# Performance work log

Hardware: AMD Instinct MI355X
Metric: run time of the kernel (lower is better)

## Reference

```python
import jax, jax.numpy as jnp
import numpy as np

B, T, C, H = 4, 2048, 768, 768  # batch, seq, embed_size, embed_size_h


def setup_inputs() -> dict:
    key = jax.random.key(0)
    ks = jax.random.split(key, 7)
    s = 1.0 / np.sqrt(C)  # torch Linear default-ish init scale
    return {
        "x": jax.random.normal(ks[0], (B, T, C), jnp.float32),
        "Wq": jax.random.normal(ks[1], (C, H), jnp.float32) * s,
        "bq": jnp.zeros((H,), jnp.float32),
        "Wk": jax.random.normal(ks[2], (C, H), jnp.float32) * s,
        "bk": jnp.zeros((H,), jnp.float32),
        "Wv": jax.random.normal(ks[3], (C, H), jnp.float32) * s,
        "bv": jnp.zeros((H,), jnp.float32),
    }


def reference(x, Wq, bq, Wk, bk, Wv, bv):
    # q,k,v: [B,T,H]
    q = x @ Wq + bq
    k = x @ Wk + bk
    v = x @ Wv + bv
    scale = jnp.asarray(H, x.dtype) ** -0.5
    # full [B,T,T] score matrix, as the original module does
    qk = jnp.einsum("btd,bsd->bts", q, k) * scale
    tril = jnp.tril(jnp.ones((T, T), x.dtype))
    qk = qk * tril
    # original quirk: masked_fill on exact zeros (covers upper triangle)
    qk = jnp.where(qk == 0, -jnp.inf, qk)
    attn = jax.nn.softmax(qk, axis=-1)  # [B,T,T]
    # note: in the source, dropout is applied to a dead value; output uses softmax directly
    return attn @ v  # [B,T,H]
```

## Files before the change

### kernel.cpp

```cpp
#include <hip/hip_runtime.h>
#include <math.h>


#define BB 4
#define TT 2048
#define CC 768

typedef __bf16 bf16_t;
typedef __bf16 bf16x8 __attribute__((ext_vector_type(8)));
typedef _Float16 half8 __attribute__((ext_vector_type(8)));
typedef float f32x4 __attribute__((ext_vector_type(4)));

__device__ __forceinline__ void async_load16(void* lds, const void* g) {
  __builtin_amdgcn_global_load_lds(
      (const __attribute__((address_space(1))) void*)g,
      (__attribute__((address_space(3))) void*)lds, 16, 0, 0);
}

__device__ __forceinline__ int swz4(int r) {
  return (r & 3) ^ ((r >> 2) & 3);
}

__device__ __forceinline__ void stage_tile(const bf16_t* __restrict__ g0,
                                           int ld, bf16_t* lds, int t) {
  int w = t >> 6, l = t & 63;
#pragma unroll
  for (int i = 0; i < 2; ++i) {
    int c = i * 256 + w * 64 + l;
    int row = c >> 2;
    int p = c & 3;
    int q = p ^ swz4(row);
    async_load16(lds + i * 2048 + w * 512,
                 g0 + row * ld + q * 8);
  }
}

__device__ __forceinline__ bf16x8 read_frag(const bf16_t* lds, int r, int q) {
  int p = q ^ swz4(r);
  return *(const bf16x8*)(lds + r * 32 + p * 8);
}

__device__ __forceinline__ void mfma_tile(const bf16_t* Ab, const bf16_t* Bb,
                                          int wr, int wc, int l,
                                          f32x4 acc[4][4]) {
  bf16x8 af[4], bfr[4];
  int q = l >> 4;
#pragma unroll
  for (int i = 0; i < 4; ++i) {
    af[i] = read_frag(Ab, wr + i * 16 + (l & 15), q);
    bfr[i] = read_frag(Bb, wc + i * 16 + (l & 15), q);
  }
#pragma unroll
  for (int mi = 0; mi < 4; ++mi)
#pragma unroll
    for (int ni = 0; ni < 4; ++ni)
      acc[mi][ni] = __builtin_amdgcn_mfma_f32_16x16x32_bf16(
          af[mi], bfr[ni], acc[mi][ni], 0, 0, 0);
}

__device__ __forceinline__ void gemm_core(const bf16_t* __restrict__ A, int lda,
                                          const bf16_t* __restrict__ B, int ldb,
                                          int kTiles, bf16_t* As0, bf16_t* As1,
                                          bf16_t* Bs0, bf16_t* Bs1,
                                          f32x4 acc[4][4]) {
  int t = threadIdx.x;
  int l = t & 63;
  int w = t >> 6;
  int wr = (w >> 1) * 64;
  int wc = (w & 1) * 64;

  stage_tile(A, lda, As0, t);
  stage_tile(B, ldb, Bs0, t);

  for (int kt = 0; kt < kTiles; kt += 2) {
    __syncthreads();
    stage_tile(A + (kt + 1) * 32, lda, As1, t);
    stage_tile(B + (kt + 1) * 32, ldb, Bs1, t);
    mfma_tile(As0, Bs0, wr, wc, l, acc);
    __syncthreads();
    if (kt + 2 < kTiles) {
      stage_tile(A + (kt + 2) * 32, lda, As0, t);
      stage_tile(B + (kt + 2) * 32, ldb, Bs0, t);
    }
    mfma_tile(As1, Bs1, wr, wc, l, acc);
  }
}


__global__ __launch_bounds__(256) void cast_x_kernel(
    const float* __restrict__ x, bf16_t* __restrict__ xbf) {
  int i = blockIdx.x * 256 + threadIdx.x;
  const float4* xin = (const float4*)x;
  float4 a = xin[i * 2];
  float4 b = xin[i * 2 + 1];
  bf16_t tmp[8];
  tmp[0] = (bf16_t)a.x; tmp[1] = (bf16_t)a.y;
  tmp[2] = (bf16_t)a.z; tmp[3] = (bf16_t)a.w;
  tmp[4] = (bf16_t)b.x; tmp[5] = (bf16_t)b.y;
  tmp[6] = (bf16_t)b.z; tmp[7] = (bf16_t)b.w;
  *(uint4*)(xbf + (size_t)i * 8) = *(const uint4*)tmp;
}

__global__ __launch_bounds__(256) void transpose_w_kernel(
    const float* __restrict__ Wq, const float* __restrict__ Wk,
    const float* __restrict__ Wv, bf16_t* __restrict__ wt) {
  int z = blockIdx.z;
  const float* W = (z == 0) ? Wq : (z == 1) ? Wk : Wv;
  bf16_t* out = wt + (size_t)z * CC * CC;
  __shared__ float tile[32][33];
  int tx = threadIdx.x;
  int ty = threadIdx.y;
  int n0 = blockIdx.x * 32;
  int c0 = blockIdx.y * 32;
#pragma unroll
  for (int k = 0; k < 4; ++k)
    tile[ty + k * 8][tx] = W[(size_t)(c0 + ty + k * 8) * CC + n0 + tx];
  __syncthreads();
#pragma unroll
  for (int k = 0; k < 4; ++k)
    out[(size_t)(n0 + ty + k * 8) * CC + c0 + tx] =
        (bf16_t)tile[tx][ty + k * 8];
}

__global__ __launch_bounds__(256) void qkv_gemm_kernel(
    const bf16_t* __restrict__ xbf, const bf16_t* __restrict__ wt,
    const float* __restrict__ bq, const float* __restrict__ bk,
    const float* __restrict__ bv, bf16_t* __restrict__ qb,
    bf16_t* __restrict__ kb, bf16_t* __restrict__ vt) {
  __shared__ bf16_t smem[16384];
  int bid = blockIdx.x;
  int work = (bid & 7) * 144 + (bid >> 3);
  int z = work / 384;
  int rw = work - z * 384;
  int m0 = (rw / 6) * 128;
  int n0 = (rw % 6) * 128;

  f32x4 acc[4][4];
#pragma unroll
  for (int i = 0; i < 4; ++i)
#pragma unroll
    for (int j = 0; j < 4; ++j) acc[i][j] = (f32x4){0.f, 0.f, 0.f, 0.f};

  const bf16_t* A = xbf + (size_t)m0 * CC;
  const bf16_t* B = wt + (size_t)z * CC * CC + (size_t)n0 * CC;
  gemm_core(A, CC, B, CC, CC / 32, smem, smem + 4096, smem + 8192,
            smem + 12288, acc);

  int t = threadIdx.x;
  int l = t & 63, w = t >> 6;
  int wr = (w >> 1) * 64, wc = (w & 1) * 64;
  const float* bias = (z == 0) ? bq : (z == 1) ? bk : bv;

  if (z < 2) {
    float scale = (z == 0) ? rsqrtf((float)CC) : 1.0f;
    bf16_t* dst = (z == 0) ? qb : kb;
#pragma unroll
    for (int mi = 0; mi < 4; ++mi) {
#pragma unroll
      for (int ni = 0; ni < 4; ++ni) {
        int col = n0 + wc + ni * 16 + (l & 15);
        int rbase = m0 + wr + mi * 16 + (l >> 4) * 4;
        float bcol = bias[col];
#pragma unroll
        for (int r = 0; r < 4; ++r) {
          float v = (acc[mi][ni][r] + bcol) * scale;
          dst[(size_t)(rbase + r) * CC + col] = (bf16_t)v;
        }
      }
    }
  } else {
    __syncthreads();
#pragma unroll
    for (int mi = 0; mi < 4; ++mi) {
#pragma unroll
      for (int ni = 0; ni < 4; ++ni) {
        int cl = wc + ni * 16 + (l & 15);
        int mlb = wr + mi * 16 + (l >> 4) * 4;
        float bcol = bias[n0 + cl];
        bf16_t t4[4];
#pragma unroll
        for (int r = 0; r < 4; ++r) t4[r] = (bf16_t)(acc[mi][ni][r] + bcol);
        int e = cl * 128 + (((mlb >> 3) ^ (cl & 15)) << 3) + (mlb & 7);
        *(uint2*)((unsigned int*)smem + (e >> 1)) = *(const uint2*)t4;
      }
    }
    __syncthreads();
    int b = m0 >> 11;
    int tt0 = m0 & (TT - 1);
#pragma unroll
    for (int g = 0; g < 8; ++g) {
      int cl = g * 16 + (t >> 4);
      int ck = t & 15;
      int phys = ck ^ (cl & 15);
      uint4 v = *(const uint4*)(smem + cl * 128 + phys * 8);
      *(uint4*)(vt + ((size_t)b * CC + n0 + cl) * TT + tt0 + ck * 8) = v;
    }
  }
}

__global__ __launch_bounds__(256, 4) void s_gemm_kernel(
    const bf16_t* __restrict__ qb, const bf16_t* __restrict__ kb,
    _Float16* __restrict__ S) {
  __shared__ bf16_t As0[4096], As1[4096], Bs0[4096], Bs1[4096];
  int bid = blockIdx.x;
  int work = (bid & 7) * 68 + (bid >> 3);
  int b = work / 136;
  int t = work - b * 136;
  int ti = (int)((sqrtf(8.f * (float)t + 1.f) - 1.f) * 0.5f);
  while ((ti + 1) * (ti + 2) / 2 <= t) ++ti;
  while (ti * (ti + 1) / 2 > t) --ti;
  int tj = t - ti * (ti + 1) / 2;
  int m0 = ti * 128, n0 = tj * 128;

  f32x4 acc[4][4];
#pragma unroll
  for (int i = 0; i < 4; ++i)
#pragma unroll
    for (int j = 0; j < 4; ++j) acc[i][j] = (f32x4){0.f, 0.f, 0.f, 0.f};

  const bf16_t* A = qb + ((size_t)b * TT + m0) * CC;
  const bf16_t* B = kb + ((size_t)b * TT + n0) * CC;
  gemm_core(A, CC, B, CC, CC / 32, As0, As1, Bs0, Bs1, acc);

  _Float16* Sb = S + (size_t)b * TT * TT;
  int l = threadIdx.x & 63, w = threadIdx.x >> 6;
  int wr = (w >> 1) * 64, wc = (w & 1) * 64;
#pragma unroll
  for (int mi = 0; mi < 4; ++mi) {
#pragma unroll
    for (int ni = 0; ni < 4; ++ni) {
      int j = n0 + wc + ni * 16 + (l & 15);
      int ibase = m0 + wr + mi * 16 + (l >> 4) * 4;
#pragma unroll
      for (int r = 0; r < 4; ++r) {
        int i = ibase + r;
        float v = acc[mi][ni][r];
        if (j > i || v == 0.0f) v = -INFINITY;
        Sb[(size_t)i * TT + j] = (_Float16)v;
      }
    }
  }
}

__global__ __launch_bounds__(256) void rowstat_kernel(
    const _Float16* __restrict__ S, bf16_t* __restrict__ P) {
  int g = blockIdx.x * 4 + (threadIdx.x >> 6);
  int b = g >> 11;
  int row = g & (TT - 1);
  int l = threadIdx.x & 63;
  const _Float16* s = S + ((size_t)b * TT + row) * TT;
  bf16_t* p = P + ((size_t)b * TT + row) * TT;
  int pe = ((row >> 7) + 1) << 7;

  float f[4][8];
#pragma unroll
  for (int c = 0; c < 4; ++c) {
    int j = (c * 64 + l) * 8;
    if (j < pe) {
      half8 h = *(const half8*)(s + j);
#pragma unroll
      for (int k = 0; k < 8; ++k) f[c][k] = (float)h[k];
    } else {
#pragma unroll
      for (int k = 0; k < 8; ++k) f[c][k] = -INFINITY;
    }
  }

  float m = f[0][0];
#pragma unroll
  for (int c = 0; c < 4; ++c)
#pragma unroll
    for (int k = 0; k < 8; ++k) m = fmaxf(m, f[c][k]);
#pragma unroll
  for (int off = 32; off > 0; off >>= 1) m = fmaxf(m, __shfl_xor(m, off));

  float e[4][8];
  float sum = 0.f;
#pragma unroll
  for (int c = 0; c < 4; ++c)
#pragma unroll
    for (int k = 0; k < 8; ++k) {
      e[c][k] = __expf(f[c][k] - m);
      sum += e[c][k];
    }
#pragma unroll
  for (int off = 32; off > 0; off >>= 1) sum += __shfl_xor(sum, off);
  float inv = 1.0f / sum;

#pragma unroll
  for (int c = 0; c < 4; ++c) {
    int j = (c * 64 + l) * 8;
    if (j < pe) {
      bf16x8 o;
#pragma unroll
      for (int k = 0; k < 8; ++k) o[k] = (bf16_t)(e[c][k] * inv);
      *(bf16x8*)(p + j) = o;
    }
  }
}

__global__ __launch_bounds__(256, 4) void o_gemm_kernel(
    const bf16_t* __restrict__ P, const bf16_t* __restrict__ vt,
    float* __restrict__ out) {
  __shared__ bf16_t As0[4096], As1[4096], Bs0[4096], Bs1[4096];
  int bid = blockIdx.x;
  int work = (bid & 7) * 48 + (bid >> 3);
  int b = work / 96;
  int rw = work - b * 96;
  int i = rw / 6, nj = rw % 6;
  int ti = (i & 1) ? ((i - 1) >> 1) : (15 - (i >> 1));
  int m0 = ti * 128, n0 = nj * 128;

  f32x4 acc[4][4];
#pragma unroll
  for (int ii = 0; ii < 4; ++ii)
#pragma unroll
    for (int j = 0; j < 4; ++j) acc[ii][j] = (f32x4){0.f, 0.f, 0.f, 0.f};

  const bf16_t* A = P + ((size_t)b * TT + m0) * TT;
  const bf16_t* B = vt + ((size_t)b * CC + n0) * TT;
  gemm_core(A, TT, B, TT, (ti + 1) * 4, As0, As1, Bs0, Bs1, acc);

  float* Ob = out + (size_t)b * TT * CC;
  int l = threadIdx.x & 63, w = threadIdx.x >> 6;
  int wr = (w >> 1) * 64, wc = (w & 1) * 64;
#pragma unroll
  for (int mi = 0; mi < 4; ++mi) {
#pragma unroll
    for (int ni = 0; ni < 4; ++ni) {
      int col = n0 + wc + ni * 16 + (l & 15);
      int ibase = m0 + wr + mi * 16 + (l >> 4) * 4;
#pragma unroll
      for (int r = 0; r < 4; ++r)
        Ob[(size_t)(ibase + r) * CC + col] = acc[mi][ni][r];
    }
  }
}

extern "C" void kernel_launch(void* const* d_in, const int* in_sizes, int n_in,
                              void* d_out, int out_size, void* d_ws,
                              size_t ws_size, hipStream_t stream) {
  const float* x = (const float*)d_in[0];
  const float* Wq = (const float*)d_in[1];
  const float* bq = (const float*)d_in[2];
  const float* Wk = (const float*)d_in[3];
  const float* bk = (const float*)d_in[4];
  const float* Wv = (const float*)d_in[5];
  const float* bv = (const float*)d_in[6];
  float* out = (float*)d_out;

  char* ws = (char*)d_ws;
  size_t off = 0;
  auto carve = [&](size_t bytes) -> char* {
    char* p = ws + off;
    off += (bytes + 255) & ~(size_t)255;
    return p;
  };
  const size_t M = (size_t)BB * TT;
  bf16_t* xbf = (bf16_t*)carve(M * CC * 2);
  bf16_t* wt  = (bf16_t*)carve(3ull * CC * CC * 2);
  bf16_t* qb  = (bf16_t*)carve(M * CC * 2);
  bf16_t* kb  = (bf16_t*)carve(M * CC * 2);
  bf16_t* vt  = (bf16_t*)carve(M * CC * 2);
  _Float16* S = (_Float16*)carve((size_t)BB * TT * TT * 2);
  bf16_t* P   = (bf16_t*)carve((size_t)BB * TT * TT * 2);
  (void)off; (void)ws_size;

  cast_x_kernel<<<(M * CC / 8 + 255) / 256, 256, 0, stream>>>(x, xbf);
  transpose_w_kernel<<<dim3(CC / 32, CC / 32, 3), dim3(32, 8, 1), 0, stream>>>(
      Wq, Wk, Wv, wt);
  qkv_gemm_kernel<<<1152, 256, 0, stream>>>(xbf, wt, bq, bk, bv, qb, kb, vt);
  s_gemm_kernel<<<544, 256, 0, stream>>>(qb, kb, S);
  rowstat_kernel<<<BB * TT / 4, 256, 0, stream>>>(S, P);
  o_gemm_kernel<<<384, 256, 0, stream>>>(P, vt, out);
}
```

Baseline: 197.9 us.

## Stage GEMM epilogues through swizzled LDS for coalesced stores; merge prep kernels

The Q/K, S and output GEMM epilogues now write accumulators into swizzled shared memory and then write them to global memory as 16-byte row-contiguous stores. Before, each lane wrote scattered 2- or 4-byte elements. The output GEMM stages its 128x128 fp32 tile in two halves so it fits in the existing LDS buffer. The x cast and weight transpose are merged into one launch to cut a kernel launch. The cost is extra barriers and LDS traffic in each epilogue.

```diff
diff --git a/kernel.cpp b/kernel.cpp
--- a/kernel.cpp
+++ b/kernel.cpp
@@ -87,39 +87,42 @@
 }
 
 
-__global__ __launch_bounds__(256) void cast_x_kernel(
-    const float* __restrict__ x, bf16_t* __restrict__ xbf) {
-  int i = blockIdx.x * 256 + threadIdx.x;
-  const float4* xin = (const float4*)x;
-  float4 a = xin[i * 2];
-  float4 b = xin[i * 2 + 1];
-  bf16_t tmp[8];
-  tmp[0] = (bf16_t)a.x; tmp[1] = (bf16_t)a.y;
-  tmp[2] = (bf16_t)a.z; tmp[3] = (bf16_t)a.w;
-  tmp[4] = (bf16_t)b.x; tmp[5] = (bf16_t)b.y;
-  tmp[6] = (bf16_t)b.z; tmp[7] = (bf16_t)b.w;
-  *(uint4*)(xbf + (size_t)i * 8) = *(const uint4*)tmp;
-}
-
-__global__ __launch_bounds__(256) void transpose_w_kernel(
-    const float* __restrict__ Wq, const float* __restrict__ Wk,
-    const float* __restrict__ Wv, bf16_t* __restrict__ wt) {
-  int z = blockIdx.z;
-  const float* W = (z == 0) ? Wq : (z == 1) ? Wk : Wv;
-  bf16_t* out = wt + (size_t)z * CC * CC;
+__global__ __launch_bounds__(256) void prep_kernel(
+    const float* __restrict__ x, const float* __restrict__ Wq,
+    const float* __restrict__ Wk, const float* __restrict__ Wv,
+    bf16_t* __restrict__ xbf, bf16_t* __restrict__ wt) {
   __shared__ float tile[32][33];
-  int tx = threadIdx.x;
-  int ty = threadIdx.y;
-  int n0 = blockIdx.x * 32;
-  int c0 = blockIdx.y * 32;
-#pragma unroll
-  for (int k = 0; k < 4; ++k)
-    tile[ty + k * 8][tx] = W[(size_t)(c0 + ty + k * 8) * CC + n0 + tx];
-  __syncthreads();
-#pragma unroll
-  for (int k = 0; k < 4; ++k)
-    out[(size_t)(n0 + ty + k * 8) * CC + c0 + tx] =
-        (bf16_t)tile[tx][ty + k * 8];
+  int bid = blockIdx.x;
+  int t = threadIdx.x;
+  if (bid < 3072) {
+    int i = bid * 256 + t;
+    const float4* xin = (const float4*)x;
+    float4 a = xin[i * 2];
+    float4 b = xin[i * 2 + 1];
+    bf16_t tmp[8];
+    tmp[0] = (bf16_t)a.x; tmp[1] = (bf16_t)a.y;
+    tmp[2] = (bf16_t)a.z; tmp[3] = (bf16_t)a.w;
+    tmp[4] = (bf16_t)b.x; tmp[5] = (bf16_t)b.y;
+    tmp[6] = (bf16_t)b.z; tmp[7] = (bf16_t)b.w;
+    *(uint4*)(xbf + (size_t)i * 8) = *(const uint4*)tmp;
+  } else {
+    int r = bid - 3072;
+    int z = r / 576;
+    r -= z * 576;
+    int by = r / 24, bx = r - by * 24;
+    const float* W = (z == 0) ? Wq : (z == 1) ? Wk : Wv;
+    bf16_t* out = wt + (size_t)z * CC * CC;
+    int tx = t & 31, ty = t >> 5;
+    int n0 = bx * 32, c0 = by * 32;
+#pragma unroll
+    for (int k = 0; k < 4; ++k)
+      tile[ty + k * 8][tx] = W[(size_t)(c0 + ty + k * 8) * CC + n0 + tx];
+    __syncthreads();
+#pragma unroll
+    for (int k = 0; k < 4; ++k)
+      out[(size_t)(n0 + ty + k * 8) * CC + c0 + tx] =
+          (bf16_t)tile[tx][ty + k * 8];
+  }
 }
 
 __global__ __launch_bounds__(256) void qkv_gemm_kernel(
@@ -150,6 +153,7 @@
   int l = t & 63, w = t >> 6;
   int wr = (w >> 1) * 64, wc = (w & 1) * 64;
   const float* bias = (z == 0) ? bq : (z == 1) ? bk : bv;
+  __syncthreads();
 
   if (z < 2) {
     float scale = (z == 0) ? rsqrtf((float)CC) : 1.0f;
@@ -158,18 +162,27 @@
     for (int mi = 0; mi < 4; ++mi) {
 #pragma unroll
       for (int ni = 0; ni < 4; ++ni) {
-        int col = n0 + wc + ni * 16 + (l & 15);
-        int rbase = m0 + wr + mi * 16 + (l >> 4) * 4;
-        float bcol = bias[col];
+        int cl = wc + ni * 16 + (l & 15);
+        int rb = wr + mi * 16 + (l >> 4) * 4;
+        float bcol = bias[n0 + cl];
 #pragma unroll
         for (int r = 0; r < 4; ++r) {
+          int row = rb + r;
           float v = (acc[mi][ni][r] + bcol) * scale;
-          dst[(size_t)(rbase + r) * CC + col] = (bf16_t)v;
+          smem[row * 128 + (((cl >> 3) ^ (row & 7)) << 3) + (cl & 7)] =
+              (bf16_t)v;
         }
       }
     }
+    __syncthreads();
+#pragma unroll
+    for (int g = 0; g < 8; ++g) {
+      int row = g * 16 + (t >> 4);
+      int ck = t & 15;
+      uint4 v = *(const uint4*)(smem + row * 128 + ((ck ^ (row & 7)) << 3));
+      *(uint4*)(dst + (size_t)(m0 + row) * CC + n0 + ck * 8) = v;
+    }
   } else {
-    __syncthreads();
 #pragma unroll
     for (int mi = 0; mi < 4; ++mi) {
 #pragma unroll
@@ -201,7 +214,7 @@
 __global__ __launch_bounds__(256, 4) void s_gemm_kernel(
     const bf16_t* __restrict__ qb, const bf16_t* __restrict__ kb,
     _Float16* __restrict__ S) {
-  __shared__ bf16_t As0[4096], As1[4096], Bs0[4096], Bs1[4096];
+  __shared__ bf16_t smem[16384];
   int bid = blockIdx.x;
   int work = (bid & 7) * 68 + (bid >> 3);
   int b = work / 136;
@@ -220,25 +233,40 @@
 
   const bf16_t* A = qb + ((size_t)b * TT + m0) * CC;
   const bf16_t* B = kb + ((size_t)b * TT + n0) * CC;
-  gemm_core(A, CC, B, CC, CC / 32, As0, As1, Bs0, Bs1, acc);
+  gemm_core(A, CC, B, CC, CC / 32, smem, smem + 4096, smem + 8192,
+            smem + 12288, acc);
 
   _Float16* Sb = S + (size_t)b * TT * TT;
-  int l = threadIdx.x & 63, w = threadIdx.x >> 6;
+  _Float16* lds = (_Float16*)smem;
+  int tid = threadIdx.x;
+  int l = tid & 63, w = tid >> 6;
   int wr = (w >> 1) * 64, wc = (w & 1) * 64;
+  __syncthreads();
 #pragma unroll
   for (int mi = 0; mi < 4; ++mi) {
 #pragma unroll
     for (int ni = 0; ni < 4; ++ni) {
-      int j = n0 + wc + ni * 16 + (l & 15);
-      int ibase = m0 + wr + mi * 16 + (l >> 4) * 4;
+      int cl = wc + ni * 16 + (l & 15);
+      int rb = wr + mi * 16 + (l >> 4) * 4;
+      int j = n0 + cl;
 #pragma unroll
       for (int r = 0; r < 4; ++r) {
-        int i = ibase + r;
+        int row = rb + r;
+        int i = m0 + row;
         float v = acc[mi][ni][r];
         if (j > i || v == 0.0f) v = -INFINITY;
-        Sb[(size_t)i * TT + j] = (_Float16)v;
+        lds[row * 128 + (((cl >> 3) ^ (row & 7)) << 3) + (cl & 7)] =
+            (_Float16)v;
       }
     }
+  }
+  __syncthreads();
+#pragma unroll
+  for (int g = 0; g < 8; ++g) {
+    int row = g * 16 + (tid >> 4);
+    int ck = tid & 15;
+    uint4 v = *(const uint4*)(lds + row * 128 + ((ck ^ (row & 7)) << 3));
+    *(uint4*)(Sb + (size_t)(m0 + row) * TT + n0 + ck * 8) = v;
   }
 }
 
@@ -302,7 +330,7 @@
 __global__ __launch_bounds__(256, 4) void o_gemm_kernel(
     const bf16_t* __restrict__ P, const bf16_t* __restrict__ vt,
     float* __restrict__ out) {
-  __shared__ bf16_t As0[4096], As1[4096], Bs0[4096], Bs1[4096];
+  __shared__ bf16_t smem[16384];
   int bid = blockIdx.x;
   int work = (bid & 7) * 48 + (bid >> 3);
   int b = work / 96;
@@ -319,20 +347,41 @@
 
   const bf16_t* A = P + ((size_t)b * TT + m0) * TT;
   const bf16_t* B = vt + ((size_t)b * CC + n0) * TT;
-  gemm_core(A, TT, B, TT, (ti + 1) * 4, As0, As1, Bs0, Bs1, acc);
+  gemm_core(A, TT, B, TT, (ti + 1) * 4, smem, smem + 4096, smem + 8192,
+            smem + 12288, acc);
 
   float* Ob = out + (size_t)b * TT * CC;
-  int l = threadIdx.x & 63, w = threadIdx.x >> 6;
+  float* lds = (float*)smem;
+  int tid = threadIdx.x;
+  int l = tid & 63, w = tid >> 6;
   int wr = (w >> 1) * 64, wc = (w & 1) * 64;
 #pragma unroll
-  for (int mi = 0; mi < 4; ++mi) {
-#pragma unroll
-    for (int ni = 0; ni < 4; ++ni) {
-      int col = n0 + wc + ni * 16 + (l & 15);
-      int ibase = m0 + wr + mi * 16 + (l >> 4) * 4;
-#pragma unroll
-      for (int r = 0; r < 4; ++r)
-        Ob[(size_t)(ibase + r) * CC + col] = acc[mi][ni][r];
+  for (int h = 0; h < 2; ++h) {
+    __syncthreads();
+    if ((w >> 1) == h) {
+#pragma unroll
+      for (int mi = 0; mi < 4; ++mi) {
+#pragma unroll
+        for (int ni = 0; ni < 4; ++ni) {
+          int cl = wc + ni * 16 + (l & 15);
+          int rb = mi * 16 + (l >> 4) * 4;
+#pragma unroll
+          for (int r = 0; r < 4; ++r) {
+            int row = rb + r;
+            lds[row * 128 + ((((cl >> 2) ^ (row & 7)) << 2) | (cl & 3))] =
+                acc[mi][ni][r];
+          }
+        }
+      }
+    }
+    __syncthreads();
+#pragma unroll
+    for (int g = 0; g < 8; ++g) {
+      int row = g * 8 + (tid >> 5);
+      int c = tid & 31;
+      uint4 v =
+          *(const uint4*)(lds + row * 128 + ((c ^ (row & 7)) << 2));
+      *(uint4*)(Ob + (size_t)(m0 + h * 64 + row) * CC + n0 + c * 4) = v;
     }
   }
 }
@@ -366,9 +415,7 @@
   bf16_t* P   = (bf16_t*)carve((size_t)BB * TT * TT * 2);
   (void)off; (void)ws_size;
 
-  cast_x_kernel<<<(M * CC / 8 + 255) / 256, 256, 0, stream>>>(x, xbf);
-  transpose_w_kernel<<<dim3(CC / 32, CC / 32, 3), dim3(32, 8, 1), 0, stream>>>(
-      Wq, Wk, Wv, wt);
+  prep_kernel<<<4800, 256, 0, stream>>>(x, Wq, Wk, Wv, xbf, wt);
   qkv_gemm_kernel<<<1152, 256, 0, stream>>>(xbf, wt, bq, bk, bv, qb, kb, vt);
   s_gemm_kernel<<<544, 256, 0, stream>>>(qb, kb, S);
   rowstat_kernel<<<BB * TT / 4, 256, 0, stream>>>(S, P);
```

Result: no change. 199.7 us (+0.9%).

## Split-K the long causal row tiles in O GEMM and add combine pass

Applied to the files above, without the earlier changes.

Row tiles in the lower half of the causal P@V GEMM, which carry the longest K ranges, are split into two K halves that run as separate workgroups, raising the grid from 384 to 576 blocks. The second half writes fp32 partials to a workspace buffer, and a new combine kernel adds them into the output. This targets load imbalance and tail effects from the triangular work distribution. The cost is an extra kernel launch, additional fp32 write/read traffic for half the output, and dropping the earlier interleaved tile ordering.

```diff
diff --git a/kernel.cpp b/kernel.cpp
--- a/kernel.cpp
+++ b/kernel.cpp
@@ -301,40 +301,84 @@
 
 __global__ __launch_bounds__(256, 4) void o_gemm_kernel(
     const bf16_t* __restrict__ P, const bf16_t* __restrict__ vt,
-    float* __restrict__ out) {
+    float* __restrict__ out, float* __restrict__ part) {
   __shared__ bf16_t As0[4096], As1[4096], Bs0[4096], Bs1[4096];
   int bid = blockIdx.x;
-  int work = (bid & 7) * 48 + (bid >> 3);
-  int b = work / 96;
-  int rw = work - b * 96;
-  int i = rw / 6, nj = rw % 6;
-  int ti = (i & 1) ? ((i - 1) >> 1) : (15 - (i >> 1));
+  int work = (bid & 7) * 72 + (bid >> 3);
+  int b = work / 144;
+  int j = work - b * 144;
+  int ti, nj, half, kstart, kt;
+  if (j < 48) {
+    ti = j / 6;
+    nj = j - ti * 6;
+    half = 0;
+    kstart = 0;
+    kt = (ti + 1) * 4;
+  } else {
+    int j2 = j - 48;
+    ti = 8 + j2 / 12;
+    int s = j2 - (ti - 8) * 12;
+    nj = s >> 1;
+    half = s & 1;
+    kt = (ti + 1) * 2;
+    kstart = half ? kt : 0;
+  }
   int m0 = ti * 128, n0 = nj * 128;
 
   f32x4 acc[4][4];
 #pragma unroll
   for (int ii = 0; ii < 4; ++ii)
 #pragma unroll
-    for (int j = 0; j < 4; ++j) acc[ii][j] = (f32x4){0.f, 0.f, 0.f, 0.f};
-
-  const bf16_t* A = P + ((size_t)b * TT + m0) * TT;
-  const bf16_t* B = vt + ((size_t)b * CC + n0) * TT;
-  gemm_core(A, TT, B, TT, (ti + 1) * 4, As0, As1, Bs0, Bs1, acc);
-
-  float* Ob = out + (size_t)b * TT * CC;
+    for (int jj = 0; jj < 4; ++jj) acc[ii][jj] = (f32x4){0.f, 0.f, 0.f, 0.f};
+
+  const bf16_t* A = P + ((size_t)b * TT + m0) * TT + kstart * 32;
+  const bf16_t* B = vt + ((size_t)b * CC + n0) * TT + kstart * 32;
+  gemm_core(A, TT, B, TT, kt, As0, As1, Bs0, Bs1, acc);
+
   int l = threadIdx.x & 63, w = threadIdx.x >> 6;
   int wr = (w >> 1) * 64, wc = (w & 1) * 64;
-#pragma unroll
-  for (int mi = 0; mi < 4; ++mi) {
-#pragma unroll
-    for (int ni = 0; ni < 4; ++ni) {
-      int col = n0 + wc + ni * 16 + (l & 15);
-      int ibase = m0 + wr + mi * 16 + (l >> 4) * 4;
-#pragma unroll
-      for (int r = 0; r < 4; ++r)
-        Ob[(size_t)(ibase + r) * CC + col] = acc[mi][ni][r];
-    }
-  }
+  if (half == 0) {
+    float* Ob = out + (size_t)b * TT * CC;
+#pragma unroll
+    for (int mi = 0; mi < 4; ++mi) {
+#pragma unroll
+      for (int ni = 0; ni < 4; ++ni) {
+        int col = n0 + wc + ni * 16 + (l & 15);
+        int ibase = m0 + wr + mi * 16 + (l >> 4) * 4;
+#pragma unroll
+        for (int r = 0; r < 4; ++r)
+          Ob[(size_t)(ibase + r) * CC + col] = acc[mi][ni][r];
+      }
+    }
+  } else {
+    float* Pb = part + (size_t)b * 1024 * CC;
+#pragma unroll
+    for (int mi = 0; mi < 4; ++mi) {
+#pragma unroll
+      for (int ni = 0; ni < 4; ++ni) {
+        int col = n0 + wc + ni * 16 + (l & 15);
+        int ibase = m0 + wr + mi * 16 + (l >> 4) * 4 - 1024;
+#pragma unroll
+        for (int r = 0; r < 4; ++r)
+          Pb[(size_t)(ibase + r) * CC + col] = acc[mi][ni][r];
+      }
+    }
+  }
+}
+
+__global__ __launch_bounds__(256) void combine_kernel(
+    const float* __restrict__ part, float* __restrict__ out) {
+  int i = blockIdx.x * 256 + threadIdx.x;
+  int b = i / (1024 * 192);
+  int rem = i - b * 1024 * 192;
+  int row = rem / 192;
+  int c4 = rem - row * 192;
+  const float4* p4 = (const float4*)part;
+  float4 pv = p4[i];
+  float4* o4 = (float4*)(out + ((size_t)b * TT + 1024 + row) * CC) + c4;
+  float4 ov = *o4;
+  ov.x += pv.x; ov.y += pv.y; ov.z += pv.z; ov.w += pv.w;
+  *o4 = ov;
 }
 
 extern "C" void kernel_launch(void* const* d_in, const int* in_sizes, int n_in,
@@ -364,6 +408,7 @@
   bf16_t* vt  = (bf16_t*)carve(M * CC * 2);
   _Float16* S = (_Float16*)carve((size_t)BB * TT * TT * 2);
   bf16_t* P   = (bf16_t*)carve((size_t)BB * TT * TT * 2);
+  float* part = (float*)carve((size_t)BB * 1024 * CC * 4);
   (void)off; (void)ws_size;
 
   cast_x_kernel<<<(M * CC / 8 + 255) / 256, 256, 0, stream>>>(x, xbf);
@@ -372,5 +417,6 @@
   qkv_gemm_kernel<<<1152, 256, 0, stream>>>(xbf, wt, bq, bk, bv, qb, kb, vt);
   s_gemm_kernel<<<544, 256, 0, stream>>>(qb, kb, S);
   rowstat_kernel<<<BB * TT / 4, 256, 0, stream>>>(S, P);
-  o_gemm_kernel<<<384, 256, 0, stream>>>(P, vt, out);
-}
+  o_gemm_kernel<<<576, 256, 0, stream>>>(P, vt, out, part);
+  combine_kernel<<<3072, 256, 0, stream>>>(part, out);
+}
```

After: 202.6 us. 2.4% more time.
